# Kernel tuning notes

Hardware: AMD Instinct MI355X
Metric: run time of the kernel (lower is better)

Reference implementation:

```python
import jax, jax.numpy as jnp
import numpy as np

B, T, D = 32, 128, 64
SPK, CELL, NCLS = 2, 64, 6
DIMS = [300, 74, 35]
BETA = 0.8            # QActivation beta
TWO_PI = 2 * 3.14     # repo uses 2*3.14, not 2*pi


def _unitary(seed, d):
    rng = np.random.default_rng(seed)
    m = rng.normal(size=(d, d)) + 1j * rng.normal(size=(d, d))
    q, _ = np.linalg.qr(m)  # exact unitary -> stable 128-step recurrence
    return jnp.asarray(q.real, jnp.float32), jnp.asarray(q.imag, jnp.float32)


def setup_inputs() -> dict:
    key = jax.random.key(0)
    ks = jax.random.split(key, 16)
    inp = {}
    for i, dm in enumerate(DIMS):
        inp[f"mod{i}"] = jax.random.normal(ks[i], (B, T, dm), jnp.float32)
        inp[f"Wp{i}"] = jax.random.normal(ks[3 + i], (dm, D), jnp.float32) / np.sqrt(dm)
        inp[f"bp{i}"] = jnp.zeros((D,), jnp.float32)
    inp["smask"] = jax.random.uniform(ks[6], (B, T, SPK), dtype=jnp.float32)
    inp["umask"] = jnp.ones((B, T), jnp.float32)
    inp["phase_table"] = jax.random.uniform(ks[7], (SPK, D), dtype=jnp.float32)
    inp["Uh_r"], inp["Uh_i"] = _unitary(1, D)
    inp["Ux_r"], inp["Ux_i"] = _unitary(2, D)
    inp["Lambda"] = jnp.asarray([0.5], jnp.float32)
    inp["K_r"] = jax.random.normal(ks[8], (D, D), jnp.float32) / np.sqrt(D)
    inp["K_i"] = jax.random.normal(ks[9], (D, D), jnp.float32) / np.sqrt(D)
    inp["W1"] = jax.random.normal(ks[10], (D, CELL), jnp.float32) / np.sqrt(D)
    inp["b1"] = jnp.zeros((CELL,), jnp.float32)
    inp["W2"] = jax.random.normal(ks[11], (CELL, NCLS), jnp.float32) / np.sqrt(CELL)
    inp["b2"] = jnp.zeros((NCLS,), jnp.float32)
    return inp


def reference(mod0, mod1, mod2, smask, umask, Wp0, bp0, Wp1, bp1, Wp2, bp2,
              phase_table, Uh_r, Uh_i, Ux_r, Ux_i, Lambda, K_r, K_i, W1, b1, W2, b2):
    d = Uh_r.shape[0]
    b, t = mod0.shape[0], mod0.shape[1]
    mods, Ws, bs = [mod0, mod1, mod2], [Wp0, Wp1, Wp2], [bp0, bp1, bp2]
    # per-modality projections + ReLU -> utterance reps (B,T,D)
    reps = [jax.nn.relu(m @ W + bb) for m, W, bb in zip(mods, Ws, bs)]
    # L2Norm -> softmax mixture weights over modalities (B,T,3)
    norms = jnp.stack([jnp.linalg.norm(r, axis=-1) for r in reps], axis=-1)
    weights = jax.nn.softmax(norms, axis=-1)
    # PositionEmbedding: speaker-conditioned phase + sinusoidal-style frequencies
    sid = jnp.argmax(smask, axis=-1)                                  # (B,T) speaker id
    freq = 1.0 / (10000.0 ** (jnp.arange(d, dtype=jnp.float32) / d))  # (D,)
    pos = jnp.arange(t, dtype=jnp.float32)[None, :, None]             # (1,T,1)
    phase = pos * freq + phase_table[sid] * TWO_PI                    # (B,T,D)
    eiphi = jnp.exp(1j * phase).astype(jnp.complex64)
    # ComplexMultiply + QOuter + QMixture fused: rho = sum_m w_m |psi_m><psi_m|
    rho = jnp.zeros((b, t, d, d), jnp.complex64)
    for m, rep in enumerate(reps):
        amp = rep / jnp.maximum(jnp.linalg.norm(rep, axis=-1, keepdims=True), 1e-12)
        psi = amp.astype(jnp.complex64) * eiphi                       # (B,T,D) pure state
        rho = rho + weights[..., m, None, None].astype(jnp.complex64) * \
              jnp.einsum('bti,btj->btij', psi, psi.conj())
    # QRNNCell recurrence (num_layers=1): h' = lam*Ux rho Ux^H + (1-lam)*Uh h Uh^H
    Uh = (Uh_r + 1j * Uh_i).astype(jnp.complex64)
    Ux = (Ux_r + 1j * Ux_i).astype(jnp.complex64)
    lam = Lambda[0].astype(jnp.complex64)
    mixed_eye = jnp.eye(d, dtype=jnp.complex64) / d

    def step(h, rho_t):
        hx = jnp.einsum('ij,bjk,lk->bil', Ux, rho_t, Ux.conj())
        hh = jnp.einsum('ij,bjk,lk->bil', Uh, h, Uh.conj())
        h_new = lam * hx + (1.0 - lam) * hh
        out = BETA * h_new + (1.0 - BETA) * mixed_eye  # QActivation (trace-preserving)
        return h_new, out

    h0 = jnp.broadcast_to(mixed_eye, (b, d, d))
    _, outs = jax.lax.scan(step, h0, jnp.swapaxes(rho, 0, 1))         # (T,B,D,D)
    rho_out = jnp.swapaxes(outs, 0, 1)                                # (B,T,D,D)
    # QMeasurement: p_j = Re( k_j^H rho k_j )
    K = (K_r + 1j * K_i).astype(jnp.complex64)
    probs = jnp.einsum('jm,btmn,jn->btj', K.conj(), rho_out, K).real  # (B,T,D)
    # SimpleNet head (dropout off in eval) + log_softmax over classes
    h1 = jax.nn.relu(probs @ W1 + b1)
    logits = jnp.tanh(h1 @ W2 + b2)                                   # (B,T,C)
    return jax.nn.log_softmax(logits, axis=2)
```

## Files before the change

kernel.cpp:

```cpp
#include <hip/hip_runtime.h>
#include <hip/hip_bf16.h>
#include <math.h>

#define DD 64
#define TT 128
#define BBATCH 32
#define BT (BBATCH*TT)
#define ND 16
#define BETA_C 0.8f
#define TWO_PI_R 6.28f
#define LG2_10000 13.28771237954945f
#define SW 328

typedef float2 cf;
typedef _Float16 f16;
typedef _Float16 half8 __attribute__((ext_vector_type(8)));
typedef _Float16 half4 __attribute__((ext_vector_type(4)));
typedef float f32x4 __attribute__((ext_vector_type(4)));

__device__ __forceinline__ void cfma(cf& acc, cf a, cf b){
  acc.x = fmaf(a.x, b.x, fmaf(-a.y, b.y, acc.x));
  acc.y = fmaf(a.x, b.y, fmaf( a.y, b.x, acc.y));
}

template<int KDIM, int KPAD>
__device__ __forceinline__ f32x4 prep_phase(
    const float* __restrict__ Wp, const float* __restrict__ modg,
    f16* sWpT, f16* sMod, int tid, int w, int l15, int l4)
{
  __syncthreads();
  constexpr int PAD = KPAD - KDIM;
  for (int i = tid; i < 64*PAD; i += 256) {
    const int r = i / PAD, p = KDIM + (i - r*PAD);
    sWpT[r*SW + p] = (f16)0.f;
  }
  for (int i = tid; i < 16*PAD; i += 256) {
    const int r = i / PAD, p = KDIM + (i - r*PAD);
    sMod[r*SW + p] = (f16)0.f;
  }
  for (int i = tid; i < KDIM*16; i += 256) {
    const int p = i >> 4, c4 = (i & 15) << 2;
    const float4 v = *(const float4*)&Wp[p*64 + c4];
    sWpT[(c4+0)*SW + p] = (f16)v.x;
    sWpT[(c4+1)*SW + p] = (f16)v.y;
    sWpT[(c4+2)*SW + p] = (f16)v.z;
    sWpT[(c4+3)*SW + p] = (f16)v.w;
  }
  for (int i = tid; i < (16*KDIM)/4; i += 256) {
    const float4 v = *(const float4*)&modg[i*4];
    const float vv[4] = {v.x, v.y, v.z, v.w};
    #pragma unroll
    for (int e2 = 0; e2 < 4; ++e2) {
      const int flat = i*4 + e2;
      const int r = flat / KDIM, p = flat - r*KDIM;
      sMod[r*SW + p] = (f16)vv[e2];
    }
  }
  __syncthreads();
  f32x4 acc = {0.f, 0.f, 0.f, 0.f};
  #pragma unroll
  for (int s = 0; s < KPAD/32; ++s) {
    const half8 a = *(const half8*)&sWpT[(w*16 + l15)*SW + s*32 + l4*8];
    const half8 b = *(const half8*)&sMod[l15*SW + s*32 + l4*8];
    acc = __builtin_amdgcn_mfma_f32_16x16x32_f16(a, b, acc, 0, 0, 0);
  }
  return acc;
}

__global__ __launch_bounds__(256) void k_front(
    const float* __restrict__ mod0, const float* __restrict__ Wp0, const float* __restrict__ bp0,
    const float* __restrict__ mod1, const float* __restrict__ Wp1, const float* __restrict__ bp1,
    const float* __restrict__ mod2, const float* __restrict__ Wp2, const float* __restrict__ bp2,
    const float* __restrict__ smask, const float* __restrict__ ptab,
    const float* __restrict__ Uhr, const float* __restrict__ Uhi,
    const float* __restrict__ Uxr, const float* __restrict__ Uxi,
    const float* __restrict__ Kr,  const float* __restrict__ Ki,
    f16* __restrict__ PsiR, f16* __restrict__ PsiI,
    f16* __restrict__ Cre, f16* __restrict__ Cim, f16* __restrict__ Cmn,
    float* __restrict__ kn)
{
  __shared__ __align__(16) char smem[65536];
  const int tid = threadIdx.x, w = tid >> 6, lane = tid & 63;
  const int l15 = lane & 15, l4 = lane >> 4;

  if (blockIdx.x < 64) {
    cf* st = (cf*)smem;
    cf (*red)[64] = (cf(*)[64])(smem + 512);
    const int j = blockIdx.x, c = lane;

    cf uh[16], ux[16];
    #pragma unroll
    for (int i = 0; i < 16; ++i) {
      const int p = w*16 + i;
      uh[i] = make_float2(Uhr[p*64 + c], Uhi[p*64 + c]);
      ux[i] = make_float2(Uxr[p*64 + c], Uxi[p*64 + c]);
    }
    if (w == 0) {
      const cf kj = make_float2(Kr[j*64 + c], -Ki[j*64 + c]);
      st[c] = kj;
      float q = fmaf(kj.x, kj.x, kj.y*kj.y);
      #pragma unroll
      for (int off = 32; off; off >>= 1) q += __shfl_xor(q, off);
      if (c == 0) kn[j] = q;
    }
    __syncthreads();

    for (int D = 0; D < ND; ++D) {
      cf cA = {0.f,0.f}, cB = {0.f,0.f}, tA = {0.f,0.f}, tB = {0.f,0.f};
      #pragma unroll
      for (int i = 0; i < 16; i += 2) {
        const cf t0 = st[w*16 + i], t1 = st[w*16 + i + 1];
        cfma(cA, t0, ux[i]); cfma(cB, t1, ux[i+1]);
        cfma(tA, t0, uh[i]); cfma(tB, t1, uh[i+1]);
      }
      red[w][c]     = make_float2(cA.x + cB.x, cA.y + cB.y);
      red[4 + w][c] = make_float2(tA.x + tB.x, tA.y + tB.y);
      __syncthreads();
      if (w == 0) {
        const cf r0 = red[0][c], r1 = red[1][c], r2 = red[2][c], r3 = red[3][c];
        const float crx = r0.x + r1.x + r2.x + r3.x;
        const float cry = r0.y + r1.y + r2.y + r3.y;
        const size_t row = (size_t)(D*64 + j)*64 + c;
        Cre[row] = (f16)crx;
        Cim[row] = (f16)cry;
        Cmn[row] = (f16)(-cry);
      } else if (w == 1) {
        const cf r0 = red[4][c], r1 = red[5][c], r2 = red[6][c], r3 = red[7][c];
        st[c] = make_float2(r0.x + r1.x + r2.x + r3.x, r0.y + r1.y + r2.y + r3.y);
      }
      __syncthreads();
    }
    return;
  }

  f16* sWpT = (f16*)smem;
  f16* sMod = (f16*)(smem + 41984);
  float* repS = (float*)(smem + 52480);
  const int bt0 = (int)(blockIdx.x - 64) * 16;

  const f32x4 a0 = prep_phase<300,320>(Wp0, mod0 + (size_t)bt0*300, sWpT, sMod, tid, w, l15, l4);
  #pragma unroll
  for (int r = 0; r < 4; ++r) {
    const int d = w*16 + l4*4 + r;
    repS[(0*16 + l15)*68 + d] = a0[r] + bp0[d];
  }
  const f32x4 a1 = prep_phase<74,96>(Wp1, mod1 + (size_t)bt0*74, sWpT, sMod, tid, w, l15, l4);
  #pragma unroll
  for (int r = 0; r < 4; ++r) {
    const int d = w*16 + l4*4 + r;
    repS[(1*16 + l15)*68 + d] = a1[r] + bp1[d];
  }
  const f32x4 a2 = prep_phase<35,64>(Wp2, mod2 + (size_t)bt0*35, sWpT, sMod, tid, w, l15, l4);
  #pragma unroll
  for (int r = 0; r < 4; ++r) {
    const int d = w*16 + l4*4 + r;
    repS[(2*16 + l15)*68 + d] = a2[r] + bp2[d];
  }
  __syncthreads();

  const int btl = tid >> 4, g = tid & 15;
  float4 v0 = *(float4*)&repS[(0*16 + btl)*68 + g*4];
  float4 v1 = *(float4*)&repS[(1*16 + btl)*68 + g*4];
  float4 v2 = *(float4*)&repS[(2*16 + btl)*68 + g*4];
  v0.x = fmaxf(v0.x, 0.f); v0.y = fmaxf(v0.y, 0.f); v0.z = fmaxf(v0.z, 0.f); v0.w = fmaxf(v0.w, 0.f);
  v1.x = fmaxf(v1.x, 0.f); v1.y = fmaxf(v1.y, 0.f); v1.z = fmaxf(v1.z, 0.f); v1.w = fmaxf(v1.w, 0.f);
  v2.x = fmaxf(v2.x, 0.f); v2.y = fmaxf(v2.y, 0.f); v2.z = fmaxf(v2.z, 0.f); v2.w = fmaxf(v2.w, 0.f);

  float q0 = v0.x*v0.x + v0.y*v0.y + v0.z*v0.z + v0.w*v0.w;
  float q1 = v1.x*v1.x + v1.y*v1.y + v1.z*v1.z + v1.w*v1.w;
  float q2 = v2.x*v2.x + v2.y*v2.y + v2.z*v2.z + v2.w*v2.w;
  #pragma unroll
  for (int off = 8; off; off >>= 1) {
    q0 += __shfl_xor(q0, off);
    q1 += __shfl_xor(q1, off);
    q2 += __shfl_xor(q2, off);
  }
  const float n0 = sqrtf(q0), n1 = sqrtf(q1), n2 = sqrtf(q2);
  const float mx = fmaxf(n0, fmaxf(n1, n2));
  const float e0 = expf(n0 - mx), e1 = expf(n1 - mx), e2 = expf(n2 - mx);
  const float inv = 1.f / (e0 + e1 + e2);
  const float sc0 = sqrtf(e0*inv) / fmaxf(n0, 1e-12f);
  const float sc1 = sqrtf(e1*inv) / fmaxf(n1, 1e-12f);
  const float sc2 = sqrtf(e2*inv) / fmaxf(n2, 1e-12f);

  const int btg = bt0 + btl;
  const int t = btg & (TT-1);
  const int sid = (smask[btg*2 + 1] > smask[btg*2]) ? 1 : 0;

  float cs[4], sn[4];
  #pragma unroll
  for (int i = 0; i < 4; ++i) {
    const int d = g*4 + i;
    const float freq = exp2f(-((float)d * (1.f/64.f)) * LG2_10000);
    const float ph = (float)t * freq + ptab[sid*64 + d] * TWO_PI_R;
    sincosf(ph, &sn[i], &cs[i]);
  }
  const float am0[4] = {v0.x*sc0, v0.y*sc0, v0.z*sc0, v0.w*sc0};
  const float am1[4] = {v1.x*sc1, v1.y*sc1, v1.z*sc1, v1.w*sc1};
  const float am2[4] = {v2.x*sc2, v2.y*sc2, v2.z*sc2, v2.w*sc2};
  half4 wr, wi;
  #pragma unroll
  for (int i = 0; i < 4; ++i) { wr[i] = (f16)(am0[i]*cs[i]); wi[i] = (f16)(am0[i]*sn[i]); }
  *(half4*)&PsiR[(size_t)(0*BT + btg)*64 + g*4] = wr;
  *(half4*)&PsiI[(size_t)(0*BT + btg)*64 + g*4] = wi;
  #pragma unroll
  for (int i = 0; i < 4; ++i) { wr[i] = (f16)(am1[i]*cs[i]); wi[i] = (f16)(am1[i]*sn[i]); }
  *(half4*)&PsiR[(size_t)(1*BT + btg)*64 + g*4] = wr;
  *(half4*)&PsiI[(size_t)(1*BT + btg)*64 + g*4] = wi;
  #pragma unroll
  for (int i = 0; i < 4; ++i) { wr[i] = (f16)(am2[i]*cs[i]); wi[i] = (f16)(am2[i]*sn[i]); }
  *(half4*)&PsiR[(size_t)(2*BT + btg)*64 + g*4] = wr;
  *(half4*)&PsiI[(size_t)(2*BT + btg)*64 + g*4] = wi;
}

#define PST 72
__global__ __launch_bounds__(256) void k_E(
    const f16* __restrict__ Cre, const f16* __restrict__ Cim, const f16* __restrict__ Cmn,
    const f16* __restrict__ PsiR, const f16* __restrict__ PsiI,
    f16* __restrict__ e16)
{
  __shared__ __align__(16) f16 sP[3][2][64][PST];
  const int bsg = blockIdx.x >> 3, cgg = blockIdx.x & 7;
  const int tid = threadIdx.x, w = tid >> 6, lane = tid & 63;
  const int l15 = lane & 15, l4 = lane >> 4;

  for (int idx = tid; idx < 512; idx += 256) {
    const int r = idx >> 3, c8 = (idx & 7) << 3;
    #pragma unroll
    for (int k = 0; k < 3; ++k) {
      const size_t g = ((size_t)(k*BT + bsg*64 + r))*64 + c8;
      *(uint4*)&sP[k][0][r][c8] = *(const uint4*)&PsiR[g];
      *(uint4*)&sP[k][1][r][c8] = *(const uint4*)&PsiI[g];
    }
  }
  __syncthreads();

  #pragma unroll
  for (int cc = 0; cc < 2; ++cc) {
    const int cg = cgg*2 + cc;
    const size_t arow = ((size_t)(cg*64 + w*16 + l15))*64 + l4*8;
    half8 aRe[2], aIm[2], aMn[2];
    aRe[0] = *(const half8*)&Cre[arow]; aRe[1] = *(const half8*)&Cre[arow + 32];
    aIm[0] = *(const half8*)&Cim[arow]; aIm[1] = *(const half8*)&Cim[arow + 32];
    aMn[0] = *(const half8*)&Cmn[arow]; aMn[1] = *(const half8*)&Cmn[arow + 32];

    #pragma unroll
    for (int ct = 0; ct < 4; ++ct) {
      f32x4 eA = {0.f,0.f,0.f,0.f};
      #pragma unroll
      for (int k = 0; k < 3; ++k) {
        f32x4 xr = {0.f,0.f,0.f,0.f}, xi = {0.f,0.f,0.f,0.f};
        #pragma unroll
        for (int kk = 0; kk < 2; ++kk) {
          const half8 bRe = *(const half8*)&sP[k][0][ct*16 + l15][l4*8 + kk*32];
          const half8 bIm = *(const half8*)&sP[k][1][ct*16 + l15][l4*8 + kk*32];
          xr = __builtin_amdgcn_mfma_f32_16x16x32_f16(aRe[kk], bRe, xr, 0, 0, 0);
          xr = __builtin_amdgcn_mfma_f32_16x16x32_f16(aMn[kk], bIm, xr, 0, 0, 0);
          xi = __builtin_amdgcn_mfma_f32_16x16x32_f16(aRe[kk], bIm, xi, 0, 0, 0);
          xi = __builtin_amdgcn_mfma_f32_16x16x32_f16(aIm[kk], bRe, xi, 0, 0, 0);
        }
        #pragma unroll
        for (int r = 0; r < 4; ++r)
          eA[r] = fmaf(xr[r], xr[r], fmaf(xi[r], xi[r], eA[r]));
      }
      half4 ev;
      #pragma unroll
      for (int r = 0; r < 4; ++r) ev[r] = (f16)eA[r];
      *(half4*)&e16[(size_t)(bsg*64 + ct*16 + l15)*1024 + cg*64 + w*16 + l4*4] = ev;
    }
  }
}

__global__ __launch_bounds__(256) void k_head(const f16* __restrict__ e16,
    const float* __restrict__ kn, const float* __restrict__ Lam,
    const float* __restrict__ W1, const float* __restrict__ b1,
    const float* __restrict__ W2, const float* __restrict__ b2,
    float* __restrict__ out)
{
  __shared__ float sW1[4096];
  __shared__ float pr[4][64];
  __shared__ float h1[4][64];
  __shared__ float lg[4][6];
  const int tid = threadIdx.x;
  const int q = tid >> 6, j = tid & 63;
  const int bt = blockIdx.x*4 + q;
  const int b = bt >> 7, t = bt & (TT-1);
  const float lam = Lam[0], om = 1.f - lam;

  for (int i = tid*4; i < 4096; i += 1024)
    *(float4*)&sW1[i] = *(const float4*)&W1[i];

  float acc = 0.f, wD = BETA_C * lam;
  const int nd = min(ND, t + 1);
  for (int D = 0; D < nd; ++D) {
    acc += wD * (float)e16[(size_t)(b*TT + t - D)*1024 + D*64 + j];
    wD *= om;
  }
  const float omt = powf(om, (float)(t + 1));
  acc += (BETA_C*omt + (1.f - BETA_C)) * kn[j] * (1.f/64.f);
  pr[q][j] = acc;
  __syncthreads();

  float a1 = b1[j];
  for (int dd = 0; dd < 64; ++dd) a1 = fmaf(pr[q][dd], sW1[dd*64 + j], a1);
  h1[q][j] = fmaxf(a1, 0.f);
  __syncthreads();

  if (j < 6) {
    float a2 = b2[j];
    for (int c = 0; c < 64; ++c) a2 = fmaf(h1[q][c], W2[c*6 + j], a2);
    lg[q][j] = tanhf(a2);
  }
  __syncthreads();
  if (j < 6) {
    float mx = -1e30f;
    #pragma unroll
    for (int n = 0; n < 6; ++n) mx = fmaxf(mx, lg[q][n]);
    float se = 0.f;
    #pragma unroll
    for (int n = 0; n < 6; ++n) se += expf(lg[q][n] - mx);
    out[bt*6 + j] = lg[q][j] - mx - logf(se);
  }
}

extern "C" void kernel_launch(void* const* d_in, const int* in_sizes, int n_in,
                              void* d_out, int out_size, void* d_ws, size_t ws_size,
                              hipStream_t stream)
{
  const float* mod0  = (const float*)d_in[0];
  const float* Wp0   = (const float*)d_in[1];
  const float* bp0   = (const float*)d_in[2];
  const float* mod1  = (const float*)d_in[3];
  const float* Wp1   = (const float*)d_in[4];
  const float* bp1   = (const float*)d_in[5];
  const float* mod2  = (const float*)d_in[6];
  const float* Wp2   = (const float*)d_in[7];
  const float* bp2   = (const float*)d_in[8];
  const float* smask = (const float*)d_in[9];
  const float* ptab  = (const float*)d_in[11];
  const float* Uhr   = (const float*)d_in[12];
  const float* Uhi   = (const float*)d_in[13];
  const float* Uxr   = (const float*)d_in[14];
  const float* Uxi   = (const float*)d_in[15];
  const float* Lam   = (const float*)d_in[16];
  const float* Kr    = (const float*)d_in[17];
  const float* Ki    = (const float*)d_in[18];
  const float* W1    = (const float*)d_in[19];
  const float* b1    = (const float*)d_in[20];
  const float* W2    = (const float*)d_in[21];
  const float* b2    = (const float*)d_in[22];

  char* ws = (char*)d_ws;
  float* kn   = (float*)(ws);
  f16*   Cre  = (f16*)  (ws + ((size_t)1024 << 10));
  f16*   Cim  = (f16*)  (ws + ((size_t)1280 << 10));
  f16*   Cmn  = (f16*)  (ws + ((size_t)1536 << 10));
  f16*   PsiR = (f16*)  (ws + ((size_t)2 << 20));
  f16*   PsiI = (f16*)  (ws + ((size_t)4 << 20));
  f16*   e16  = (f16*)  (ws + ((size_t)6 << 20));
  if (ws_size < ((size_t)16 << 20)) return;

  k_front<<<320, 256, 0, stream>>>(mod0, Wp0, bp0, mod1, Wp1, bp1, mod2, Wp2, bp2,
                                   smask, ptab, Uhr, Uhi, Uxr, Uxi, Kr, Ki,
                                   PsiR, PsiI, Cre, Cim, Cmn, kn);
  k_E<<<512, 256, 0, stream>>>(Cre, Cim, Cmn, PsiR, PsiI, e16);
  k_head<<<1024, 256, 0, stream>>>(e16, kn, Lam, W1, b1, W2, b2, (float*)d_out);
}
```

Baseline: 47.00 us.

## Double-buffer Psi tiles in k_E, stage outputs through LDS, cheaper pow

The k_E kernel no longer loads all three modality Psi tiles up front. It double-buffers them in shared memory, prefetching the next modality into registers while MFMAs run on the current one, which shrinks LDS use and lets the loads overlap compute. The loop is reordered so A fragments for both column groups and all eight accumulators stay in registers. The output is transposed through LDS so e16 is written with coalesced 16-byte stores, and powf is replaced with exp2(log2) in the head kernel. The cost is more register pressure and extra barriers.

```diff
diff --git a/kernel.cpp b/kernel.cpp
--- a/kernel.cpp
+++ b/kernel.cpp
@@ -219,55 +219,91 @@
     const f16* __restrict__ PsiR, const f16* __restrict__ PsiI,
     f16* __restrict__ e16)
 {
-  __shared__ __align__(16) f16 sP[3][2][64][PST];
+  __shared__ __align__(16) f16 sP[2][2][64][PST];
   const int bsg = blockIdx.x >> 3, cgg = blockIdx.x & 7;
   const int tid = threadIdx.x, w = tid >> 6, lane = tid & 63;
   const int l15 = lane & 15, l4 = lane >> 4;
 
-  for (int idx = tid; idx < 512; idx += 256) {
-    const int r = idx >> 3, c8 = (idx & 7) << 3;
-    #pragma unroll
-    for (int k = 0; k < 3; ++k) {
-      const size_t g = ((size_t)(k*BT + bsg*64 + r))*64 + c8;
-      *(uint4*)&sP[k][0][r][c8] = *(const uint4*)&PsiR[g];
-      *(uint4*)&sP[k][1][r][c8] = *(const uint4*)&PsiI[g];
-    }
-  }
-  __syncthreads();
-
+  half8 aRe[2][2], aIm[2][2], aMn[2][2];
   #pragma unroll
   for (int cc = 0; cc < 2; ++cc) {
-    const int cg = cgg*2 + cc;
-    const size_t arow = ((size_t)(cg*64 + w*16 + l15))*64 + l4*8;
-    half8 aRe[2], aIm[2], aMn[2];
-    aRe[0] = *(const half8*)&Cre[arow]; aRe[1] = *(const half8*)&Cre[arow + 32];
-    aIm[0] = *(const half8*)&Cim[arow]; aIm[1] = *(const half8*)&Cim[arow + 32];
-    aMn[0] = *(const half8*)&Cmn[arow]; aMn[1] = *(const half8*)&Cmn[arow + 32];
-
-    #pragma unroll
-    for (int ct = 0; ct < 4; ++ct) {
-      f32x4 eA = {0.f,0.f,0.f,0.f};
+    const size_t arow = ((size_t)((cgg*2 + cc)*64 + w*16 + l15))*64 + l4*8;
+    aRe[cc][0] = *(const half8*)&Cre[arow]; aRe[cc][1] = *(const half8*)&Cre[arow + 32];
+    aIm[cc][0] = *(const half8*)&Cim[arow]; aIm[cc][1] = *(const half8*)&Cim[arow + 32];
+    aMn[cc][0] = *(const half8*)&Cmn[arow]; aMn[cc][1] = *(const half8*)&Cmn[arow + 32];
+  }
+
+  const int r0s = tid >> 3, c8s = (tid & 7) << 3;
+  const int r1s = (tid + 256) >> 3;
+  {
+    const size_t g0 = ((size_t)(0*BT + bsg*64 + r0s))*64 + c8s;
+    const size_t g1 = ((size_t)(0*BT + bsg*64 + r1s))*64 + c8s;
+    *(uint4*)&sP[0][0][r0s][c8s] = *(const uint4*)&PsiR[g0];
+    *(uint4*)&sP[0][1][r0s][c8s] = *(const uint4*)&PsiI[g0];
+    *(uint4*)&sP[0][0][r1s][c8s] = *(const uint4*)&PsiR[g1];
+    *(uint4*)&sP[0][1][r1s][c8s] = *(const uint4*)&PsiI[g1];
+  }
+
+  f32x4 eAcc[2][4];
+  #pragma unroll
+  for (int cc = 0; cc < 2; ++cc)
+    #pragma unroll
+    for (int ct = 0; ct < 4; ++ct) eAcc[cc][ct] = (f32x4){0.f,0.f,0.f,0.f};
+
+  #pragma unroll
+  for (int k = 0; k < 3; ++k) {
+    uint4 nR0, nI0, nR1, nI1;
+    if (k < 2) {
+      const size_t g0 = ((size_t)((k+1)*BT + bsg*64 + r0s))*64 + c8s;
+      const size_t g1 = ((size_t)((k+1)*BT + bsg*64 + r1s))*64 + c8s;
+      nR0 = *(const uint4*)&PsiR[g0];
+      nI0 = *(const uint4*)&PsiI[g0];
+      nR1 = *(const uint4*)&PsiR[g1];
+      nI1 = *(const uint4*)&PsiI[g1];
+    }
+    __syncthreads();
+    const int kb = k & 1;
+    #pragma unroll
+    for (int cc = 0; cc < 2; ++cc) {
       #pragma unroll
-      for (int k = 0; k < 3; ++k) {
+      for (int ct = 0; ct < 4; ++ct) {
         f32x4 xr = {0.f,0.f,0.f,0.f}, xi = {0.f,0.f,0.f,0.f};
         #pragma unroll
         for (int kk = 0; kk < 2; ++kk) {
-          const half8 bRe = *(const half8*)&sP[k][0][ct*16 + l15][l4*8 + kk*32];
-          const half8 bIm = *(const half8*)&sP[k][1][ct*16 + l15][l4*8 + kk*32];
-          xr = __builtin_amdgcn_mfma_f32_16x16x32_f16(aRe[kk], bRe, xr, 0, 0, 0);
-          xr = __builtin_amdgcn_mfma_f32_16x16x32_f16(aMn[kk], bIm, xr, 0, 0, 0);
-          xi = __builtin_amdgcn_mfma_f32_16x16x32_f16(aRe[kk], bIm, xi, 0, 0, 0);
-          xi = __builtin_amdgcn_mfma_f32_16x16x32_f16(aIm[kk], bRe, xi, 0, 0, 0);
+          const half8 bRe = *(const half8*)&sP[kb][0][ct*16 + l15][l4*8 + kk*32];
+          const half8 bIm = *(const half8*)&sP[kb][1][ct*16 + l15][l4*8 + kk*32];
+          xr = __builtin_amdgcn_mfma_f32_16x16x32_f16(aRe[cc][kk], bRe, xr, 0, 0, 0);
+          xr = __builtin_amdgcn_mfma_f32_16x16x32_f16(aMn[cc][kk], bIm, xr, 0, 0, 0);
+          xi = __builtin_amdgcn_mfma_f32_16x16x32_f16(aRe[cc][kk], bIm, xi, 0, 0, 0);
+          xi = __builtin_amdgcn_mfma_f32_16x16x32_f16(aIm[cc][kk], bRe, xi, 0, 0, 0);
         }
         #pragma unroll
         for (int r = 0; r < 4; ++r)
-          eA[r] = fmaf(xr[r], xr[r], fmaf(xi[r], xi[r], eA[r]));
+          eAcc[cc][ct][r] = fmaf(xr[r], xr[r], fmaf(xi[r], xi[r], eAcc[cc][ct][r]));
       }
-      half4 ev;
+    }
+    if (k < 2) {
+      const int nb = kb ^ 1;
+      *(uint4*)&sP[nb][0][r0s][c8s] = nR0;
+      *(uint4*)&sP[nb][1][r0s][c8s] = nI0;
+      *(uint4*)&sP[nb][0][r1s][c8s] = nR1;
+      *(uint4*)&sP[nb][1][r1s][c8s] = nI1;
+    }
+  }
+
+  f16* sE = (f16*)sP;
+  #pragma unroll
+  for (int cc = 0; cc < 2; ++cc) {
+    __syncthreads();
+    #pragma unroll
+    for (int ct = 0; ct < 4; ++ct)
       #pragma unroll
-      for (int r = 0; r < 4; ++r) ev[r] = (f16)eA[r];
-      *(half4*)&e16[(size_t)(bsg*64 + ct*16 + l15)*1024 + cg*64 + w*16 + l4*4] = ev;
-    }
+      for (int r = 0; r < 4; ++r)
+        sE[(ct*16 + l15)*PST + w*16 + l4*4 + r] = (f16)eAcc[cc][ct][r];
+    __syncthreads();
+    const int cg = cgg*2 + cc;
+    *(uint4*)&e16[((size_t)(bsg*64 + r0s))*1024 + cg*64 + c8s] = *(const uint4*)&sE[r0s*PST + c8s];
+    *(uint4*)&e16[((size_t)(bsg*64 + r1s))*1024 + cg*64 + c8s] = *(const uint4*)&sE[r1s*PST + c8s];
   }
 }
 
@@ -296,7 +332,7 @@
     acc += wD * (float)e16[(size_t)(b*TT + t - D)*1024 + D*64 + j];
     wD *= om;
   }
-  const float omt = powf(om, (float)(t + 1));
+  const float omt = exp2f((float)(t + 1) * log2f(om));
   acc += (BETA_C*omt + (1.f - BETA_C)) * kn[j] * (1.f/64.f);
   pr[q][j] = acc;
   __syncthreads();
```

Measured after the change: 46.16 us. Within noise of the previous version (-1.8%).
